# Kernel optimization log

Measured on AMD Instinct MI355X. Metric: run time of the kernel, lower is better.

## Reference

```python
import jax, jax.numpy as jnp
import numpy as np

B, T, N, E, H, L, K = 2, 32, 256, 1024, 16, 2, 256
MAXLEN = 512  # RelativeMultiheadAttention max_seq_len default
SCALES = (1, 2, 4)
TAU = 1.0


def setup_inputs() -> dict:
    key = jax.random.key(0)
    ks = jax.random.split(key, 9)
    s = 0.02
    A = 2 * L  # [layer0-spatial, layer0-temporal, layer1-spatial, layer1-temporal]
    return {
        "x": jax.random.normal(ks[0], (B, T, N, E), jnp.float32),
        "attn_wq": jax.random.normal(ks[1], (A, E, E), jnp.float32) * s,
        "attn_bq": jnp.zeros((A, E), jnp.float32),
        "attn_wk": jax.random.normal(ks[2], (A, E, E), jnp.float32) * s,
        "attn_bk": jnp.zeros((A, E), jnp.float32),
        "attn_wv": jax.random.normal(ks[3], (A, E, E), jnp.float32) * s,
        "attn_bv": jnp.zeros((A, E), jnp.float32),
        "attn_wd": jax.random.normal(ks[4], (A, E, E), jnp.float32) * s,
        "attn_bd": jnp.zeros((A, E), jnp.float32),
        "rel_bias": jax.random.normal(ks[5], (A, 2 * MAXLEN - 1, H), jnp.float32) * s,
        "sel_w": jax.random.normal(ks[6], (E, K), jnp.float32) * s,
        "sel_b": jnp.zeros((K,), jnp.float32),
    }


def _rel_attn(x, wq, bq, wk, bk, wv, bv, wd, bd, rb):
    # x: [Bx, S, E]; rb: [2*MAXLEN-1, H]
    Bx, S, _ = x.shape
    D = E // H
    q = (x @ wq + bq).reshape(Bx, S, H, D)
    k = (x @ wk + bk).reshape(Bx, S, H, D)
    v = (x @ wv + bv).reshape(Bx, S, H, D)
    scores = jnp.einsum('bshd,bthd->bhst', q, k) / jnp.sqrt(jnp.asarray(D, x.dtype))
    pos = jnp.arange(S)
    idx = pos[None, :] - pos[:, None] + (MAXLEN - 1)  # [S, S]
    bias = rb[idx]  # [S, S, H] gathered relative-position bias
    scores = scores + bias.transpose(2, 0, 1)[None]
    w = jax.nn.softmax(scores, axis=-1)
    ctx = jnp.einsum('bhst,bthd->bshd', w, v).reshape(Bx, S, E)
    return ctx @ wd + bd


def reference(x, attn_wq, attn_bq, attn_wk, attn_bk, attn_wv, attn_bv,
              attn_wd, attn_bd, rel_bias, sel_w, sel_b):
    h = x
    for l in range(L):
        # spatial attention over tokens within each frame
        i = 2 * l
        hs = h.reshape(B * T, N, E)
        hs = _rel_attn(hs, attn_wq[i], attn_bq[i], attn_wk[i], attn_bk[i],
                       attn_wv[i], attn_bv[i], attn_wd[i], attn_bd[i], rel_bias[i])
        # temporal attention across frames per spatial location
        j = 2 * l + 1
        ht = hs.reshape(B, T, N, E).transpose(0, 2, 1, 3).reshape(B * N, T, E)
        ht = _rel_attn(ht, attn_wq[j], attn_bq[j], attn_wk[j], attn_bk[j],
                       attn_wv[j], attn_bv[j], attn_wd[j], attn_bd[j], rel_bias[j])
        h = ht.reshape(B, N, T, E).transpose(0, 2, 1, 3)
    # DifferentiableTokenSelection: softmax-weighted pooling into K tokens
    flat = h.reshape(B, T * N, E)
    sc = flat @ sel_w + sel_b  # [B, T*N, K]
    wts = jax.nn.softmax(sc / TAU, axis=1)
    sel = jnp.einsum('bmk,bme->bke', wts, flat)  # [B, K, E]
    # multi-scale average pooling (kernel==stride==scale), concat along tokens
    outs = [sel.reshape(B, K // s, s, E).mean(axis=2) for s in SCALES]
    return jnp.concatenate(outs, axis=1)  # [B, K + K//2 + K//4, E]
```

## Files before the change

### kernel.cpp

```cpp
#include <hip/hip_runtime.h>
#include <stdint.h>


using f16x8 = __attribute__((ext_vector_type(8))) _Float16;
using f16x4 = __attribute__((ext_vector_type(4))) _Float16;
using f32x4 = __attribute__((ext_vector_type(4))) float;

__device__ __forceinline__ int tmap_dev(int m) {
    int bx = m >> 5;
    int s  = m & 31;
    int b  = bx >> 8;
    int n  = bx & 255;
    return (((b << 5) + s) << 8) + n;
}

__device__ __forceinline__ void load16(const _Float16* g, _Float16* l)
{
    __builtin_amdgcn_global_load_lds(
        (const __attribute__((address_space(1))) unsigned int*)g,
        (__attribute__((address_space(3))) unsigned int*)l,
        16, 0, 0);
}

__device__ __forceinline__ void split_f16(float v, _Float16& h, _Float16& l)
{
    h = (_Float16)v;
    l = (_Float16)(v - (float)h);
}

__global__ __launch_bounds__(256)
void conv_act(const float* __restrict__ src, _Float16* __restrict__ dh,
              _Float16* __restrict__ dl, int m_off)
{
    int idx = blockIdx.x * 256 + threadIdx.x;
    int e = idx << 3;
    int ml = e >> 10, col = e & 1023;
    const float* s = src + (size_t)(m_off + ml) * 1024 + col;
    float4 a = *(const float4*)s;
    float4 b = *(const float4*)(s + 4);
    float vv[8] = {a.x, a.y, a.z, a.w, b.x, b.y, b.z, b.w};
    f16x8 vh, vl;
    #pragma unroll
    for (int r = 0; r < 8; r++) {
        _Float16 h, l;
        split_f16(vv[r], h, l);
        vh[r] = h; vl[r] = l;
    }
    *(f16x8*)(dh + (size_t)ml * 1024 + col) = vh;
    *(f16x8*)(dl + (size_t)ml * 1024 + col) = vl;
}

__global__ __launch_bounds__(256)
void conv_wT(const float* __restrict__ W, _Float16* __restrict__ Th,
             _Float16* __restrict__ Tl, int ncols)
{
    __shared__ float Ls[64][65];
    const int n0 = blockIdx.x * 64, k0 = blockIdx.y * 64;
    const int t = threadIdx.x;
    const int kk = t >> 4, nn = (t & 15) << 2;
    #pragma unroll
    for (int i = 0; i < 4; i++) {
        float4 v = *(const float4*)(W + (size_t)(k0 + kk + 16 * i) * ncols + n0 + nn);
        Ls[kk + 16 * i][nn + 0] = v.x; Ls[kk + 16 * i][nn + 1] = v.y;
        Ls[kk + 16 * i][nn + 2] = v.z; Ls[kk + 16 * i][nn + 3] = v.w;
    }
    __syncthreads();
    const int nl = t >> 4, kc = (t & 15) << 2;
    #pragma unroll
    for (int i = 0; i < 4; i++) {
        int n = nl + 16 * i;
        f16x4 hh, ll;
        #pragma unroll
        for (int c = 0; c < 4; c++) {
            _Float16 h, l;
            split_f16(Ls[kc + c][n], h, l);
            hh[c] = h; ll[c] = l;
        }
        *(f16x4*)(Th + (size_t)(n0 + n) * 1024 + k0 + kc) = hh;
        *(f16x4*)(Tl + (size_t)(n0 + n) * 1024 + k0 + kc) = ll;
    }
}

template<int EPI>
__device__ __forceinline__ void gemm_core(
    const _Float16* __restrict__ Ah, const _Float16* __restrict__ Al,
    const _Float16* __restrict__ Wh, const _Float16* __restrict__ Wl,
    const float* __restrict__ bias,
    float* __restrict__ C, _Float16* __restrict__ Ch, _Float16* __restrict__ Cl,
    int ldc, int map_in, int m_off_in, int map_out, int m_off_out,
    int n0, int m0)
{
    __shared__ uint32_t smem_u[8512];
    _Float16* smem = (_Float16*)smem_u;
    _Float16* sAh = smem;
    _Float16* sAl = smem + 4096;
    _Float16* sBh = smem + 8192;
    _Float16* sBl = smem + 12288;

    const int tid = threadIdx.x;
    const int lane = tid & 63;
    const int wv = tid >> 6;
    const int fm = (wv >> 1) << 6;
    const int fn = (wv & 1) << 6;
    const int lm = lane & 15, lq = lane >> 4;

    f32x4 acc[4][4] = {};

    const int srow = tid >> 2;
    const int skc  = (tid & 3) << 3;
    const int gm0 = m_off_in + m0 + srow;
    const int gm1 = gm0 + 64;
    const int r0 = map_in ? tmap_dev(gm0) : gm0;
    const int r1 = map_in ? tmap_dev(gm1) : gm1;
    const _Float16* gAh0 = Ah + (size_t)r0 * 1024 + skc;
    const _Float16* gAh1 = Ah + (size_t)r1 * 1024 + skc;
    const _Float16* gAl0 = Al + (size_t)r0 * 1024 + skc;
    const _Float16* gAl1 = Al + (size_t)r1 * 1024 + skc;
    const _Float16* gB0 = Wh + (size_t)(n0 + srow) * 1024 + skc;
    const _Float16* gB1 = Wl + (size_t)(n0 + srow) * 1024 + skc;
    const int lo = tid << 3;

    for (int k0 = 0; k0 < 1024; k0 += 32) {
        load16(gAh0 + k0, sAh + lo);
        load16(gAh1 + k0, sAh + lo + 2048);
        load16(gAl0 + k0, sAl + lo);
        load16(gAl1 + k0, sAl + lo + 2048);
        load16(gB0 + k0,         sBh + lo);
        load16(gB0 + k0 + 65536, sBh + lo + 2048);
        load16(gB1 + k0,         sBl + lo);
        load16(gB1 + k0 + 65536, sBl + lo + 2048);
        __syncthreads();

        f16x8 ah[4], al[4], bh[4], bl[4];
        #pragma unroll
        for (int i = 0; i < 4; i++) {
            int ra = (fm + i * 16 + lm) * 32 + lq * 8;
            ah[i] = *(const f16x8*)(sAh + ra);
            al[i] = *(const f16x8*)(sAl + ra);
            int rb_ = (fn + i * 16 + lm) * 32 + lq * 8;
            bh[i] = *(const f16x8*)(sBh + rb_);
            bl[i] = *(const f16x8*)(sBl + rb_);
        }
        #pragma unroll
        for (int i = 0; i < 4; i++)
            #pragma unroll
            for (int j = 0; j < 4; j++) {
                acc[i][j] = __builtin_amdgcn_mfma_f32_16x16x32_f16(ah[i], bh[j], acc[i][j], 0, 0, 0);
                acc[i][j] = __builtin_amdgcn_mfma_f32_16x16x32_f16(ah[i], bl[j], acc[i][j], 0, 0, 0);
                acc[i][j] = __builtin_amdgcn_mfma_f32_16x16x32_f16(al[i], bh[j], acc[i][j], 0, 0, 0);
            }
        __syncthreads();
    }

    if (EPI == 0 || EPI == 1) {
        #pragma unroll
        for (int j = 0; j < 4; j++) {
            int n = n0 + fn + j * 16 + lm;
            float bb = bias[n];
            #pragma unroll
            for (int i = 0; i < 4; i++) {
                #pragma unroll
                for (int r = 0; r < 4; r++) {
                    int gm = m_off_out + m0 + fm + i * 16 + lq * 4 + r;
                    int row = map_out ? tmap_dev(gm) : gm;
                    float v = acc[i][j][r] + bb;
                    if (EPI == 0) {
                        C[(size_t)row * ldc + n] = v;
                    } else {
                        _Float16 h, l;
                        split_f16(v, h, l);
                        Ch[(size_t)row * 1024 + n] = h;
                        Cl[(size_t)row * 1024 + n] = l;
                    }
                }
            }
        }
    } else {
        const int fmh = fm >> 6;
        #pragma unroll
        for (int mh = 0; mh < 2; mh++) {
            __syncthreads();
            if (fmh == mh) {
                #pragma unroll
                for (int j = 0; j < 4; j++) {
                    int n = fn + j * 16 + lm;
                    float bb = bias[n0 + n];
                    #pragma unroll
                    for (int i = 0; i < 4; i++) {
                        #pragma unroll
                        for (int r = 0; r < 4; r++) {
                            float v = acc[i][j][r] + bb;
                            _Float16 h, l;
                            split_f16(v, h, l);
                            uint32_t ph = (uint32_t)__builtin_bit_cast(unsigned short, h);
                            uint32_t pl = (uint32_t)__builtin_bit_cast(unsigned short, l);
                            smem_u[(i * 16 + lq * 4 + r) * 133 + n] = ph | (pl << 16);
                        }
                    }
                }
            }
            __syncthreads();
            #pragma unroll
            for (int g = 0; g < 8; g++) {
                int u = tid + g * 256;
                int nn = u >> 4;
                int mg = (u & 15) << 2;
                uint32_t p0 = smem_u[(mg + 0) * 133 + nn];
                uint32_t p1 = smem_u[(mg + 1) * 133 + nn];
                uint32_t p2 = smem_u[(mg + 2) * 133 + nn];
                uint32_t p3 = smem_u[(mg + 3) * 133 + nn];
                f16x4 hh, ll;
                hh[0] = __builtin_bit_cast(_Float16, (unsigned short)(p0 & 0xffff));
                hh[1] = __builtin_bit_cast(_Float16, (unsigned short)(p1 & 0xffff));
                hh[2] = __builtin_bit_cast(_Float16, (unsigned short)(p2 & 0xffff));
                hh[3] = __builtin_bit_cast(_Float16, (unsigned short)(p3 & 0xffff));
                ll[0] = __builtin_bit_cast(_Float16, (unsigned short)(p0 >> 16));
                ll[1] = __builtin_bit_cast(_Float16, (unsigned short)(p1 >> 16));
                ll[2] = __builtin_bit_cast(_Float16, (unsigned short)(p2 >> 16));
                ll[3] = __builtin_bit_cast(_Float16, (unsigned short)(p3 >> 16));
                size_t off = (size_t)(n0 + nn) * 8192 + (m0 + mh * 64 + mg);
                *(f16x4*)(Ch + off) = hh;
                *(f16x4*)(Cl + off) = ll;
            }
        }
    }
}

__global__ __launch_bounds__(256, 2)
void gemm_f16s_f32(const _Float16* __restrict__ Ah, const _Float16* __restrict__ Al,
                   int map_in, int m_off_in,
                   const _Float16* __restrict__ Wh, const _Float16* __restrict__ Wl,
                   const float* __restrict__ bias, float* __restrict__ C, int ldc,
                   int map_out, int m_off_out)
{
    gemm_core<0>(Ah, Al, Wh, Wl, bias, C, nullptr, nullptr, ldc,
                 map_in, m_off_in, map_out, m_off_out,
                 blockIdx.x * 128, blockIdx.y * 128);
}

__global__ __launch_bounds__(256, 2)
void gemm_f16s_h(const _Float16* __restrict__ Ah, const _Float16* __restrict__ Al,
                 int map_in, int m_off_in,
                 const _Float16* __restrict__ Wh, const _Float16* __restrict__ Wl,
                 const float* __restrict__ bias,
                 _Float16* __restrict__ Ch, _Float16* __restrict__ Cl,
                 int map_out, int m_off_out)
{
    gemm_core<1>(Ah, Al, Wh, Wl, bias, nullptr, Ch, Cl, 1024,
                 map_in, m_off_in, map_out, m_off_out,
                 blockIdx.x * 128, blockIdx.y * 128);
}

__global__ __launch_bounds__(256, 2)
void gemm_qkvsplit(const _Float16* __restrict__ Ah, const _Float16* __restrict__ Al,
                   int map_in, int m_off_in,
                   const _Float16* __restrict__ WTh, const _Float16* __restrict__ WTl,
                   const float* __restrict__ bq, const float* __restrict__ bk,
                   const float* __restrict__ bv,
                   _Float16* __restrict__ Qh, _Float16* __restrict__ Ql,
                   _Float16* __restrict__ Kh, _Float16* __restrict__ Kl,
                   _Float16* __restrict__ VTh, _Float16* __restrict__ VTl)
{
    const int z = blockIdx.z;
    const _Float16* wh = WTh + (size_t)z * 1048576;
    const _Float16* wl = WTl + (size_t)z * 1048576;
    if (z == 0)
        gemm_core<1>(Ah, Al, wh, wl, bq, nullptr, Qh, Ql, 1024,
                     map_in, m_off_in, 0, 0, blockIdx.x * 128, blockIdx.y * 128);
    else if (z == 1)
        gemm_core<1>(Ah, Al, wh, wl, bk, nullptr, Kh, Kl, 1024,
                     map_in, m_off_in, 0, 0, blockIdx.x * 128, blockIdx.y * 128);
    else
        gemm_core<3>(Ah, Al, wh, wl, bv, nullptr, VTh, VTl, 0,
                     map_in, m_off_in, 0, 0, blockIdx.x * 128, blockIdx.y * 128);
}

__global__ __launch_bounds__(256, 2)
void attn_s_m(const _Float16* __restrict__ Qh, const _Float16* __restrict__ Ql,
              const _Float16* __restrict__ Kh, const _Float16* __restrict__ Kl,
              const _Float16* __restrict__ VTh, const _Float16* __restrict__ VTl,
              const float* __restrict__ RB,
              _Float16* __restrict__ Ch, _Float16* __restrict__ Cl)
{
    __shared__ _Float16 sKh[2048], sKl[2048];
    __shared__ _Float16 sVh[2560], sVl[2560];
    __shared__ _Float16 sPh[4][2560], sPl[4][2560];
    __shared__ float Bt[512];

    const int tid = threadIdx.x;
    const int lane = tid & 63;
    const int w = tid >> 6;
    const int lm = lane & 15, lq = lane >> 4;
    const int frame = blockIdx.x;
    const int h = blockIdx.y;
    const int rowbase = frame * 256;

    #pragma unroll
    for (int l = 0; l < 2; l++) {
        int idx = tid + l * 256;
        if (idx < 511) Bt[idx] = RB[(size_t)(256 + idx) * 16 + h];
    }

    f16x8 qbh[4][2], qbl[4][2];
    #pragma unroll
    for (int st = 0; st < 4; st++)
        #pragma unroll
        for (int kk = 0; kk < 2; kk++) {
            size_t qo = (size_t)(rowbase + w * 64 + st * 16 + lm) * 1024
                        + h * 64 + kk * 32 + lq * 8;
            qbh[st][kk] = *(const f16x8*)(Qh + qo);
            qbl[st][kk] = *(const f16x8*)(Ql + qo);
        }

    f32x4 cacc[4][4] = {};
    float lsum[4] = {0.f, 0.f, 0.f, 0.f};
    _Float16* Ph = sPh[w];
    _Float16* Pl = sPl[w];

    const int skrow = tid >> 3, skd = (tid & 7) << 3;
    const int svrow = tid >> 2, svj = (tid & 3) << 3;

    for (int jc = 0; jc < 8; jc++) {
        __syncthreads();
        {
            size_t ko = (size_t)(rowbase + jc * 32 + skrow) * 1024 + h * 64 + skd;
            *(f16x8*)(sKh + skrow * 64 + skd) = *(const f16x8*)(Kh + ko);
            *(f16x8*)(sKl + skrow * 64 + skd) = *(const f16x8*)(Kl + ko);
            size_t vo = (size_t)(h * 64 + svrow) * 8192 + rowbase + jc * 32 + svj;
            *(f16x8*)(sVh + svrow * 40 + svj) = *(const f16x8*)(VTh + vo);
            *(f16x8*)(sVl + svrow * 40 + svj) = *(const f16x8*)(VTl + vo);
        }
        __syncthreads();

        f32x4 sacc[2][4] = {};
        #pragma unroll
        for (int jt = 0; jt < 2; jt++) {
            f16x8 kah[2], kal[2];
            #pragma unroll
            for (int kk = 0; kk < 2; kk++) {
                int ra = (jt * 16 + lm) * 64 + kk * 32 + lq * 8;
                kah[kk] = *(const f16x8*)(sKh + ra);
                kal[kk] = *(const f16x8*)(sKl + ra);
            }
            #pragma unroll
            for (int st = 0; st < 4; st++)
                #pragma unroll
                for (int kk = 0; kk < 2; kk++) {
                    sacc[jt][st] = __builtin_amdgcn_mfma_f32_16x16x32_f16(kah[kk], qbh[st][kk], sacc[jt][st], 0, 0, 0);
                    sacc[jt][st] = __builtin_amdgcn_mfma_f32_16x16x32_f16(kah[kk], qbl[st][kk], sacc[jt][st], 0, 0, 0);
                    sacc[jt][st] = __builtin_amdgcn_mfma_f32_16x16x32_f16(kal[kk], qbh[st][kk], sacc[jt][st], 0, 0, 0);
                }
        }

        #pragma unroll
        for (int jt = 0; jt < 2; jt++)
            #pragma unroll
            for (int st = 0; st < 4; st++) {
                f16x4 p4h, p4l;
                #pragma unroll
                for (int r = 0; r < 4; r++) {
                    int j = jc * 32 + jt * 16 + lq * 4 + r;
                    int s = w * 64 + st * 16 + lm;
                    float p = __expf(sacc[jt][st][r] * 0.125f + Bt[j - s + 255]);
                    lsum[st] += p;
                    _Float16 hp, lp;
                    split_f16(p, hp, lp);
                    p4h[r] = hp; p4l[r] = lp;
                }
                int pa = (st * 16 + lm) * 40 + jt * 16 + lq * 4;
                *(f16x4*)(Ph + pa) = p4h;
                *(f16x4*)(Pl + pa) = p4l;
            }

        #pragma unroll
        for (int st = 0; st < 4; st++) {
            int pb = (st * 16 + lm) * 40 + lq * 8;
            f16x8 pbh = *(const f16x8*)(Ph + pb);
            f16x8 pbl = *(const f16x8*)(Pl + pb);
            #pragma unroll
            for (int dt = 0; dt < 4; dt++) {
                int va = (dt * 16 + lm) * 40 + lq * 8;
                f16x8 vah = *(const f16x8*)(sVh + va);
                f16x8 val = *(const f16x8*)(sVl + va);
                cacc[dt][st] = __builtin_amdgcn_mfma_f32_16x16x32_f16(vah, pbh, cacc[dt][st], 0, 0, 0);
                cacc[dt][st] = __builtin_amdgcn_mfma_f32_16x16x32_f16(vah, pbl, cacc[dt][st], 0, 0, 0);
                cacc[dt][st] = __builtin_amdgcn_mfma_f32_16x16x32_f16(val, pbh, cacc[dt][st], 0, 0, 0);
            }
        }
    }

    float inv[4];
    #pragma unroll
    for (int st = 0; st < 4; st++) {
        float t = lsum[st];
        t += __shfl_xor(t, 16);
        t += __shfl_xor(t, 32);
        inv[st] = 1.0f / t;
    }

    #pragma unroll
    for (int st = 0; st < 4; st++)
        #pragma unroll
        for (int dt = 0; dt < 4; dt++) {
            f16x4 oh, ol;
            #pragma unroll
            for (int r = 0; r < 4; r++) {
                _Float16 hp, lp;
                split_f16(cacc[dt][st][r] * inv[st], hp, lp);
                oh[r] = hp; ol[r] = lp;
            }
            size_t oo = (size_t)(rowbase + w * 64 + st * 16 + lm) * 1024
                        + h * 64 + dt * 16 + lq * 4;
            *(f16x4*)(Ch + oo) = oh;
            *(f16x4*)(Cl + oo) = ol;
        }
}

__global__ __launch_bounds__(256, 2)
void attn_t_m(const _Float16* __restrict__ Qh, const _Float16* __restrict__ Ql,
              const _Float16* __restrict__ Kh, const _Float16* __restrict__ Kl,
              const _Float16* __restrict__ VTh, const _Float16* __restrict__ VTl,
              const float* __restrict__ RB,
              _Float16* __restrict__ Ch, _Float16* __restrict__ Cl)
{
    __shared__ _Float16 sPh[4][1280], sPl[4][1280];
    __shared__ float Bt[64];

    const int tid = threadIdx.x;
    const int lane = tid & 63;
    const int w = tid >> 6;
    const int lm = lane & 15, lq = lane >> 4;
    const int h = blockIdx.y;
    const int bx = blockIdx.x * 4 + w;
    const int rowbase = bx * 32;

    if (tid < 63) Bt[tid] = RB[(size_t)(480 + tid) * 16 + h];
    __syncthreads();

    f16x8 qbh[2][2], qbl[2][2];
    #pragma unroll
    for (int st = 0; st < 2; st++)
        #pragma unroll
        for (int kk = 0; kk < 2; kk++) {
            size_t qo = (size_t)(rowbase + st * 16 + lm) * 1024 + h * 64 + kk * 32 + lq * 8;
            qbh[st][kk] = *(const f16x8*)(Qh + qo);
            qbl[st][kk] = *(const f16x8*)(Ql + qo);
        }

    f32x4 sacc[2][2] = {};
    #pragma unroll
    for (int jt = 0; jt < 2; jt++) {
        f16x8 kah[2], kal[2];
        #pragma unroll
        for (int kk = 0; kk < 2; kk++) {
            size_t ko = (size_t)(rowbase + jt * 16 + lm) * 1024 + h * 64 + kk * 32 + lq * 8;
            kah[kk] = *(const f16x8*)(Kh + ko);
            kal[kk] = *(const f16x8*)(Kl + ko);
        }
        #pragma unroll
        for (int st = 0; st < 2; st++)
            #pragma unroll
            for (int kk = 0; kk < 2; kk++) {
                sacc[jt][st] = __builtin_amdgcn_mfma_f32_16x16x32_f16(kah[kk], qbh[st][kk], sacc[jt][st], 0, 0, 0);
                sacc[jt][st] = __builtin_amdgcn_mfma_f32_16x16x32_f16(kah[kk], qbl[st][kk], sacc[jt][st], 0, 0, 0);
                sacc[jt][st] = __builtin_amdgcn_mfma_f32_16x16x32_f16(kal[kk], qbh[st][kk], sacc[jt][st], 0, 0, 0);
            }
    }

    float lsum[2] = {0.f, 0.f};
    _Float16* Ph = sPh[w];
    _Float16* Pl = sPl[w];
    #pragma unroll
    for (int jt = 0; jt < 2; jt++)
        #pragma unroll
        for (int st = 0; st < 2; st++) {
            f16x4 p4h, p4l;
            #pragma unroll
            for (int r = 0; r < 4; r++) {
                int j = jt * 16 + lq * 4 + r;
                int s = st * 16 + lm;
                float p = __expf(sacc[jt][st][r] * 0.125f + Bt[j - s + 31]);
                lsum[st] += p;
                _Float16 hp, lp;
                split_f16(p, hp, lp);
                p4h[r] = hp; p4l[r] = lp;
            }
            int pa = (st * 16 + lm) * 40 + jt * 16 + lq * 4;
            *(f16x4*)(Ph + pa) = p4h;
            *(f16x4*)(Pl + pa) = p4l;
        }

    f16x8 vah[4], val[4];
    #pragma unroll
    for (int dt = 0; dt < 4; dt++) {
        size_t vo = (size_t)(h * 64 + dt * 16 + lm) * 8192 + rowbase + lq * 8;
        vah[dt] = *(const f16x8*)(VTh + vo);
        val[dt] = *(const f16x8*)(VTl + vo);
    }
    f32x4 cacc[4][2] = {};
    #pragma unroll
    for (int st = 0; st < 2; st++) {
        int pb = (st * 16 + lm) * 40 + lq * 8;
        f16x8 pbh = *(const f16x8*)(Ph + pb);
        f16x8 pbl = *(const f16x8*)(Pl + pb);
        #pragma unroll
        for (int dt = 0; dt < 4; dt++) {
            cacc[dt][st] = __builtin_amdgcn_mfma_f32_16x16x32_f16(vah[dt], pbh, cacc[dt][st], 0, 0, 0);
            cacc[dt][st] = __builtin_amdgcn_mfma_f32_16x16x32_f16(vah[dt], pbl, cacc[dt][st], 0, 0, 0);
            cacc[dt][st] = __builtin_amdgcn_mfma_f32_16x16x32_f16(val[dt], pbh, cacc[dt][st], 0, 0, 0);
        }
    }

    float inv[2];
    #pragma unroll
    for (int st = 0; st < 2; st++) {
        float t = lsum[st];
        t += __shfl_xor(t, 16);
        t += __shfl_xor(t, 32);
        inv[st] = 1.0f / t;
    }

    #pragma unroll
    for (int st = 0; st < 2; st++)
        #pragma unroll
        for (int dt = 0; dt < 4; dt++) {
            f16x4 oh, ol;
            #pragma unroll
            for (int r = 0; r < 4; r++) {
                _Float16 hp, lp;
                split_f16(cacc[dt][st][r] * inv[st], hp, lp);
                oh[r] = hp; ol[r] = lp;
            }
            size_t oo = (size_t)(rowbase + st * 16 + lm) * 1024 + h * 64 + dt * 16 + lq * 4;
            *(f16x4*)(Ch + oo) = oh;
            *(f16x4*)(Cl + oo) = ol;
        }
}

__global__ __launch_bounds__(256)
void colsum_part_kernel(const float* __restrict__ SC, float* __restrict__ P)
{
    int bid = blockIdx.x;
    int b = bid >> 7, chunk = bid & 127;
    int base = b * 8192 + chunk * 64;
    int k = threadIdx.x;
    float sum = 0.0f;
    for (int r = 0; r < 64; r++)
        sum += __expf(SC[(size_t)(base + r) * 256 + k]);
    P[(size_t)bid * 256 + k] = sum;
}

__global__ __launch_bounds__(256)
void colsum_reduce_kernel(const float* __restrict__ P, float* __restrict__ CS)
{
    int b = blockIdx.x;
    int k = threadIdx.x;
    float s = 0.0f;
    for (int c = 0; c < 128; c++)
        s += P[(size_t)(b * 128 + c) * 256 + k];
    CS[b * 256 + k] = s;
}

__global__ __launch_bounds__(256)
void trans_wts(const float* __restrict__ SC, const float* __restrict__ CS,
               _Float16* __restrict__ Th, _Float16* __restrict__ Tl)
{
    __shared__ float L[64][65];
    const int mt = blockIdx.x * 64;
    const int kt = blockIdx.y * 64;
    const int b  = mt >> 13;
    const int ml = mt & 8191;
    const int tid = threadIdx.x;
    #pragma unroll
    for (int l = 0; l < 4; l++) {
        int idx = tid + 256 * l;
        int r = idx >> 4, c4 = (idx & 15) << 2;
        float4 v = *(const float4*)(SC + (size_t)(mt + r) * 256 + kt + c4);
        L[r][c4 + 0] = __expf(v.x); L[r][c4 + 1] = __expf(v.y);
        L[r][c4 + 2] = __expf(v.z); L[r][c4 + 3] = __expf(v.w);
    }
    __syncthreads();
    #pragma unroll
    for (int l = 0; l < 4; l++) {
        int idx = tid + 256 * l;
        int rk = idx >> 4, c4 = (idx & 15) << 2;
        float inv = 1.0f / CS[b * 256 + kt + rk];
        f16x4 hh, ll;
        #pragma unroll
        for (int u = 0; u < 4; u++) {
            _Float16 h, l2;
            split_f16(L[c4 + u][rk] * inv, h, l2);
            hh[u] = h; ll[u] = l2;
        }
        size_t o = ((size_t)b * 256 + kt + rk) * 8192 + ml + c4;
        *(f16x4*)(Th + o) = hh;
        *(f16x4*)(Tl + o) = ll;
    }
}

__global__ __launch_bounds__(256)
void trans_f16(const _Float16* __restrict__ Sh, const _Float16* __restrict__ Sl,
               _Float16* __restrict__ Th, _Float16* __restrict__ Tl)
{
    __shared__ _Float16 L[64][72];
    const int mt = blockIdx.x * 64, et = blockIdx.y * 64;
    const _Float16* S = blockIdx.z ? Sl : Sh;
    _Float16* T = blockIdx.z ? Tl : Th;
    const int tid = threadIdx.x;
    #pragma unroll
    for (int l = 0; l < 2; l++) {
        int v = tid * 2 + l;
        int r = v >> 3, c8 = (v & 7) << 3;
        *(f16x8*)&L[r][c8] = *(const f16x8*)(S + (size_t)(mt + r) * 1024 + et + c8);
    }
    __syncthreads();
    #pragma unroll
    for (int l = 0; l < 2; l++) {
        int v = tid * 2 + l;
        int r = v >> 3, c8 = (v & 7) << 3;
        f16x8 o;
        #pragma unroll
        for (int u = 0; u < 8; u++) o[u] = L[c8 + u][r];
        *(f16x8*)(T + (size_t)(et + r) * 16384 + mt + c8) = o;
    }
}

__global__ __launch_bounds__(256, 2)
void gemm_selm(const _Float16* __restrict__ Wth, const _Float16* __restrict__ Wtl,
               const _Float16* __restrict__ Hth, const _Float16* __restrict__ Htl,
               float* __restrict__ P)
{
    __shared__ _Float16 sAh[4096], sAl[4096], sBh[4096], sBl[4096];
    const int tid = threadIdx.x;
    const int lane = tid & 63;
    const int wv = tid >> 6;
    const int fm = (wv >> 1) << 6;
    const int fn = (wv & 1) << 6;
    const int lm = lane & 15, lq = lane >> 4;
    const int n0 = blockIdx.x * 128;
    const int m0 = blockIdx.y * 128;
    const int z  = blockIdx.z;
    const int b = z >> 3, sp = z & 7;

    f32x4 acc[4][4] = {};

    const int srow = tid >> 2;
    const int skc  = (tid & 3) << 3;
    const _Float16* gAh0 = Wth + ((size_t)b * 256 + m0 + srow) * 8192 + sp * 1024 + skc;
    const _Float16* gAl0 = Wtl + ((size_t)b * 256 + m0 + srow) * 8192 + sp * 1024 + skc;
    const _Float16* gB0 = Hth + (size_t)(n0 + srow) * 16384 + b * 8192 + sp * 1024 + skc;
    const _Float16* gB1 = Htl + (size_t)(n0 + srow) * 16384 + b * 8192 + sp * 1024 + skc;
    const int lo = tid << 3;

    for (int k0 = 0; k0 < 1024; k0 += 32) {
        load16(gAh0 + k0,          sAh + lo);
        load16(gAh0 + k0 + 524288, sAh + lo + 2048);
        load16(gAl0 + k0,          sAl + lo);
        load16(gAl0 + k0 + 524288, sAl + lo + 2048);
        load16(gB0 + k0,           sBh + lo);
        load16(gB0 + k0 + 1048576, sBh + lo + 2048);
        load16(gB1 + k0,           sBl + lo);
        load16(gB1 + k0 + 1048576, sBl + lo + 2048);
        __syncthreads();

        f16x8 ah[4], al[4], bh[4], bl[4];
        #pragma unroll
        for (int i = 0; i < 4; i++) {
            int ra = (fm + i * 16 + lm) * 32 + lq * 8;
            ah[i] = *(const f16x8*)(sAh + ra);
            al[i] = *(const f16x8*)(sAl + ra);
            int rb_ = (fn + i * 16 + lm) * 32 + lq * 8;
            bh[i] = *(const f16x8*)(sBh + rb_);
            bl[i] = *(const f16x8*)(sBl + rb_);
        }
        #pragma unroll
        for (int i = 0; i < 4; i++)
            #pragma unroll
            for (int j = 0; j < 4; j++) {
                acc[i][j] = __builtin_amdgcn_mfma_f32_16x16x32_f16(ah[i], bh[j], acc[i][j], 0, 0, 0);
                acc[i][j] = __builtin_amdgcn_mfma_f32_16x16x32_f16(ah[i], bl[j], acc[i][j], 0, 0, 0);
                acc[i][j] = __builtin_amdgcn_mfma_f32_16x16x32_f16(al[i], bh[j], acc[i][j], 0, 0, 0);
            }
        __syncthreads();
    }

    float* Pz = P + (size_t)z * 262144;
    #pragma unroll
    for (int j = 0; j < 4; j++) {
        int n = n0 + fn + j * 16 + lm;
        #pragma unroll
        for (int i = 0; i < 4; i++)
            #pragma unroll
            for (int r = 0; r < 4; r++) {
                int k = m0 + fm + i * 16 + lq * 4 + r;
                Pz[(size_t)k * 1024 + n] = acc[i][j][r];
            }
    }
}

__global__ __launch_bounds__(256)
void sel_reduce(const float* __restrict__ P, float* __restrict__ SEL)
{
    int idx4 = blockIdx.x * 256 + threadIdx.x;
    int e = idx4 << 2;
    int b = e >> 18;
    int rest = e & 262143;
    const float* p = P + (size_t)(b * 8) * 262144 + rest;
    float4 acc = {0.f, 0.f, 0.f, 0.f};
    #pragma unroll
    for (int s = 0; s < 8; s++) {
        float4 v = *(const float4*)(p + (size_t)s * 262144);
        acc.x += v.x; acc.y += v.y; acc.z += v.z; acc.w += v.w;
    }
    *(float4*)(SEL + e) = acc;
}

__global__ __launch_bounds__(256)
void pool_kernel(const float* __restrict__ SEL, float* __restrict__ out)
{
    int i4 = blockIdx.x * 256 + threadIdx.x;
    int e  = i4 << 2;
    int row = e >> 10;
    int b = row / 448;
    int r = row - b * 448;
    int c = e & 1023;
    const float* sb = SEL + (size_t)b * (256 * 1024);
    float4 o;
    if (r < 256) {
        o = *(const float4*)(sb + (size_t)r * 1024 + c);
    } else if (r < 384) {
        int r2 = (r - 256) * 2;
        float4 x0 = *(const float4*)(sb + (size_t)r2 * 1024 + c);
        float4 x1 = *(const float4*)(sb + (size_t)(r2 + 1) * 1024 + c);
        o.x = 0.5f * (x0.x + x1.x); o.y = 0.5f * (x0.y + x1.y);
        o.z = 0.5f * (x0.z + x1.z); o.w = 0.5f * (x0.w + x1.w);
    } else {
        int r4 = (r - 384) * 4;
        float4 x0 = *(const float4*)(sb + (size_t)(r4 + 0) * 1024 + c);
        float4 x1 = *(const float4*)(sb + (size_t)(r4 + 1) * 1024 + c);
        float4 x2 = *(const float4*)(sb + (size_t)(r4 + 2) * 1024 + c);
        float4 x3 = *(const float4*)(sb + (size_t)(r4 + 3) * 1024 + c);
        o.x = 0.25f * (x0.x + x1.x + x2.x + x3.x);
        o.y = 0.25f * (x0.y + x1.y + x2.y + x3.y);
        o.z = 0.25f * (x0.z + x1.z + x2.z + x3.z);
        o.w = 0.25f * (x0.w + x1.w + x2.w + x3.w);
    }
    *(float4*)(out + e) = o;
}

extern "C" void kernel_launch(void* const* d_in, const int* in_sizes, int n_in,
                              void* d_out, int out_size, void* d_ws, size_t ws_size,
                              hipStream_t stream)
{
    const float* x    = (const float*)d_in[0];
    const float* wq   = (const float*)d_in[1];
    const float* bq   = (const float*)d_in[2];
    const float* wk   = (const float*)d_in[3];
    const float* bk   = (const float*)d_in[4];
    const float* wv   = (const float*)d_in[5];
    const float* bv   = (const float*)d_in[6];
    const float* wd   = (const float*)d_in[7];
    const float* bd   = (const float*)d_in[8];
    const float* rb   = (const float*)d_in[9];
    const float* selw = (const float*)d_in[10];
    const float* selb = (const float*)d_in[11];
    float* out = (float*)d_out;

    float* base = (float*)d_ws;
    _Float16* Hh  = (_Float16*)base;
    _Float16* Hl  = Hh + 16777216;
    _Float16* Qh  = (_Float16*)(base + 16777216);
    _Float16* Ql  = Qh + 8388608;
    _Float16* Kh  = Ql + 8388608;
    _Float16* Kl  = Kh + 8388608;
    _Float16* VTh = (_Float16*)(base + 33554432);
    _Float16* VTl = VTh + 8388608;
    _Float16* CXh = (_Float16*)(base + 41943040);
    _Float16* CXl = CXh + 8388608;
    _Float16* WTh = (_Float16*)(base + 50331648);
    _Float16* WTl = WTh + 4194304;
    _Float16* Ah  = (_Float16*)(base + 54525952);
    _Float16* Al  = Ah + 8388608;
    float* SC   = (float*)Qh;
    float* Pp   = (float*)Kh;
    float* SEL  = (float*)Kl;
    float* PART = SEL + 524288;
    float* CSUM = PART + 65536;
    _Float16* WTTh = CXh;
    _Float16* WTTl = CXl;
    _Float16* HTh  = Ah;
    _Float16* HTl  = VTh;

    const dim3 blk(256);

    for (int a = 0; a < 4; a++) {
        const int mi = (a & 1);
        const size_t wo = (size_t)a * 1048576;
        const int bo = a * 1024;
        const float* rba = rb + (size_t)a * 1023 * 16;

        conv_wT<<<dim3(16, 16), blk, 0, stream>>>(wq + wo, WTh,           WTl,           1024);
        conv_wT<<<dim3(16, 16), blk, 0, stream>>>(wk + wo, WTh + 1048576, WTl + 1048576, 1024);
        conv_wT<<<dim3(16, 16), blk, 0, stream>>>(wv + wo, WTh + 2097152, WTl + 2097152, 1024);
        conv_wT<<<dim3(16, 16), blk, 0, stream>>>(wd + wo, WTh + 3145728, WTl + 3145728, 1024);

        for (int c = 0; c < 2; c++) {
            const int mo = c * 8192;
            const _Float16 *sH, *sL;
            int sm, so;
            if (a == 0) {
                conv_act<<<4096, blk, 0, stream>>>(x, Ah, Al, mo);
                sH = Ah; sL = Al; sm = 0; so = 0;
            } else {
                sH = Hh; sL = Hl; sm = mi; so = mo;
            }
            gemm_qkvsplit<<<dim3(8, 64, 3), blk, 0, stream>>>(
                sH, sL, sm, so, WTh, WTl, bq + bo, bk + bo, bv + bo,
                Qh, Ql, Kh, Kl, VTh, VTl);
            if (mi == 0)
                attn_s_m<<<dim3(32, 16), blk, 0, stream>>>(Qh, Ql, Kh, Kl, VTh, VTl, rba, CXh, CXl);
            else
                attn_t_m<<<dim3(64, 16), blk, 0, stream>>>(Qh, Ql, Kh, Kl, VTh, VTl, rba, CXh, CXl);
            gemm_f16s_h<<<dim3(8, 64), blk, 0, stream>>>(
                CXh, CXl, 0, 0, WTh + 3145728, WTl + 3145728, bd + bo, Hh, Hl, mi, mo);
        }
    }

    conv_wT<<<dim3(4, 16), blk, 0, stream>>>(selw, WTh, WTl, 256);
    gemm_f16s_f32<<<dim3(2, 128), blk, 0, stream>>>(
        Hh, Hl, 0, 0, WTh, WTl, selb, SC, 256, 0, 0);
    colsum_part_kernel<<<256, blk, 0, stream>>>(SC, PART);
    colsum_reduce_kernel<<<2, blk, 0, stream>>>(PART, CSUM);
    trans_wts<<<dim3(256, 4), blk, 0, stream>>>(SC, CSUM, WTTh, WTTl);
    trans_f16<<<dim3(256, 16, 2), blk, 0, stream>>>(Hh, Hl, HTh, HTl);
    gemm_selm<<<dim3(8, 2, 16), blk, 0, stream>>>(WTTh, WTTl, HTh, HTl, Pp);
    sel_reduce<<<512, blk, 0, stream>>>(Pp, SEL);
    pool_kernel<<<896, blk, 0, stream>>>(SEL, out);
}
```

Measured before the change: 2.507 ms.

## Use 256x128 GEMM tiles with 512 threads, triple buffering, and swizzled block order

Replaces the 128x128 split-fp16 GEMMs used for the QKV and output projections with a new 256x128 tile core run by 512 threads (8 waves). The core uses three-stage global-to-LDS pipelining with XOR-swizzled LDS layout and s_setprio around the MFMA blocks. A 1D grid with a remapped block index groups tiles for better L2 reuse of the A and W panels. The larger tile cuts redundant A/W loads per output, at the cost of much more LDS per block (144KB), which may limit occupancy to one block per CU despite launch_bounds(512,2).

Result: faster. 2.124 ms (-15.3%).

```diff
diff --git a/kernel.cpp b/kernel.cpp
--- a/kernel.cpp
+++ b/kernel.cpp
@@ -238,41 +238,208 @@
                  blockIdx.x * 128, blockIdx.y * 128);
 }
 
-__global__ __launch_bounds__(256, 2)
-void gemm_f16s_h(const _Float16* __restrict__ Ah, const _Float16* __restrict__ Al,
+template<int EPI>
+__device__ __forceinline__ void gemm256_core(
+    uint32_t* __restrict__ smem_u,
+    const _Float16* __restrict__ Ah, const _Float16* __restrict__ Al,
+    const _Float16* __restrict__ Wh, const _Float16* __restrict__ Wl,
+    const float* __restrict__ bias,
+    _Float16* __restrict__ Ch, _Float16* __restrict__ Cl,
+    int map_in, int m_off_in, int map_out, int m_off_out,
+    int n0, int m0)
+{
+    _Float16* S = (_Float16*)smem_u;
+    const int tid  = threadIdx.x;
+    const int lane = tid & 63;
+    const int wv = tid >> 6;
+    const int wm = wv >> 1;
+    const int fm = wm << 6;
+    const int fn = (wv & 1) << 6;
+    const int lm = lane & 15, lq = lane >> 4;
+    const int ko = ((lq ^ ((lm >> 1) & 3)) << 3);
+
+    f32x4 acc[4][4] = {};
+
+    const int srow = tid >> 2;
+    const int scol = (((tid & 3) ^ ((tid >> 3) & 3)) << 3);
+    const int gm0 = m_off_in + m0 + srow;
+    const int gm1 = gm0 + 128;
+    const int r0 = map_in ? tmap_dev(gm0) : gm0;
+    const int r1 = map_in ? tmap_dev(gm1) : gm1;
+    const _Float16* gAh0 = Ah + (size_t)r0 * 1024 + scol;
+    const _Float16* gAh1 = Ah + (size_t)r1 * 1024 + scol;
+    const _Float16* gAl0 = Al + (size_t)r0 * 1024 + scol;
+    const _Float16* gAl1 = Al + (size_t)r1 * 1024 + scol;
+    const _Float16* gBh  = Wh + (size_t)(n0 + srow) * 1024 + scol;
+    const _Float16* gBl  = Wl + (size_t)(n0 + srow) * 1024 + scol;
+    const int lo = tid << 3;
+
+    auto stage = [&](int t, int b) {
+        const int k0 = t << 5;
+        _Float16* d = S + b * 24576;
+        load16(gAh0 + k0, d + lo);
+        load16(gAh1 + k0, d + 4096  + lo);
+        load16(gAl0 + k0, d + 8192  + lo);
+        load16(gAl1 + k0, d + 12288 + lo);
+        load16(gBh  + k0, d + 16384 + lo);
+        load16(gBl  + k0, d + 20480 + lo);
+    };
+
+    auto kstep = [&](int t, int cb, int sb, bool last) {
+        if (last) asm volatile("s_waitcnt vmcnt(0) lgkmcnt(0)" ::: "memory");
+        else      asm volatile("s_waitcnt vmcnt(6) lgkmcnt(0)" ::: "memory");
+        __builtin_amdgcn_s_barrier();
+        if (sb >= 0) stage(t + 2, sb);
+
+        const _Float16* c = S + cb * 24576;
+        f16x8 ah[4], al[4], bh[4], bl[4];
+        #pragma unroll
+        for (int i = 0; i < 4; i++) {
+            int ra = (fm + i * 16 + lm) * 32 + ko;
+            ah[i] = *(const f16x8*)(c + ra);
+            al[i] = *(const f16x8*)(c + 8192 + ra);
+            int rb = (fn + i * 16 + lm) * 32 + ko;
+            bh[i] = *(const f16x8*)(c + 16384 + rb);
+            bl[i] = *(const f16x8*)(c + 20480 + rb);
+        }
+        __builtin_amdgcn_s_setprio(1);
+        #pragma unroll
+        for (int i = 0; i < 4; i++)
+            #pragma unroll
+            for (int j = 0; j < 4; j++) {
+                acc[i][j] = __builtin_amdgcn_mfma_f32_16x16x32_f16(ah[i], bh[j], acc[i][j], 0, 0, 0);
+                acc[i][j] = __builtin_amdgcn_mfma_f32_16x16x32_f16(ah[i], bl[j], acc[i][j], 0, 0, 0);
+                acc[i][j] = __builtin_amdgcn_mfma_f32_16x16x32_f16(al[i], bh[j], acc[i][j], 0, 0, 0);
+            }
+        __builtin_amdgcn_s_setprio(0);
+    };
+
+    stage(0, 0);
+    stage(1, 1);
+    #pragma unroll 1
+    for (int tt = 0; tt < 30; tt += 3) {
+        kstep(tt + 0, 0, 2, false);
+        kstep(tt + 1, 1, 0, false);
+        kstep(tt + 2, 2, 1, false);
+    }
+    kstep(30, 0, -1, false);
+    kstep(31, 1, -1, true);
+
+    if (EPI == 1) {
+        #pragma unroll
+        for (int j = 0; j < 4; j++) {
+            int n = n0 + fn + j * 16 + lm;
+            float bb = bias[n];
+            #pragma unroll
+            for (int i = 0; i < 4; i++) {
+                #pragma unroll
+                for (int r = 0; r < 4; r++) {
+                    int gm = m_off_out + m0 + fm + i * 16 + lq * 4 + r;
+                    int row = map_out ? tmap_dev(gm) : gm;
+                    float v = acc[i][j][r] + bb;
+                    _Float16 h, l;
+                    split_f16(v, h, l);
+                    Ch[(size_t)row * 1024 + n] = h;
+                    Cl[(size_t)row * 1024 + n] = l;
+                }
+            }
+        }
+    } else {
+        #pragma unroll 1
+        for (int q = 0; q < 4; q++) {
+            __syncthreads();
+            if (wm == q) {
+                #pragma unroll
+                for (int j = 0; j < 4; j++) {
+                    int ncol = fn + j * 16 + lm;
+                    float bb = bias[n0 + ncol];
+                    #pragma unroll
+                    for (int i = 0; i < 4; i++) {
+                        #pragma unroll
+                        for (int r = 0; r < 4; r++) {
+                            float v = acc[i][j][r] + bb;
+                            _Float16 h, l;
+                            split_f16(v, h, l);
+                            uint32_t ph = (uint32_t)__builtin_bit_cast(unsigned short, h);
+                            uint32_t pl = (uint32_t)__builtin_bit_cast(unsigned short, l);
+                            smem_u[(i * 16 + lq * 4 + r) * 129 + ncol] = ph | (pl << 16);
+                        }
+                    }
+                }
+            }
+            __syncthreads();
+            #pragma unroll
+            for (int g = 0; g < 4; g++) {
+                int u = tid + g * 512;
+                int nn = u >> 4;
+                int mg = (u & 15) << 2;
+                uint32_t p0 = smem_u[(mg + 0) * 129 + nn];
+                uint32_t p1 = smem_u[(mg + 1) * 129 + nn];
+                uint32_t p2 = smem_u[(mg + 2) * 129 + nn];
+                uint32_t p3 = smem_u[(mg + 3) * 129 + nn];
+                f16x4 hh, ll;
+                hh[0] = __builtin_bit_cast(_Float16, (unsigned short)(p0 & 0xffff));
+                hh[1] = __builtin_bit_cast(_Float16, (unsigned short)(p1 & 0xffff));
+                hh[2] = __builtin_bit_cast(_Float16, (unsigned short)(p2 & 0xffff));
+                hh[3] = __builtin_bit_cast(_Float16, (unsigned short)(p3 & 0xffff));
+                ll[0] = __builtin_bit_cast(_Float16, (unsigned short)(p0 >> 16));
+                ll[1] = __builtin_bit_cast(_Float16, (unsigned short)(p1 >> 16));
+                ll[2] = __builtin_bit_cast(_Float16, (unsigned short)(p2 >> 16));
+                ll[3] = __builtin_bit_cast(_Float16, (unsigned short)(p3 >> 16));
+                size_t off = (size_t)(n0 + nn) * 8192 + (m0 + q * 64 + mg);
+                *(f16x4*)(Ch + off) = hh;
+                *(f16x4*)(Cl + off) = ll;
+            }
+        }
+    }
+}
+
+__global__ __launch_bounds__(512, 2)
+void gemm_qkv256(const _Float16* __restrict__ Ah, const _Float16* __restrict__ Al,
                  int map_in, int m_off_in,
-                 const _Float16* __restrict__ Wh, const _Float16* __restrict__ Wl,
-                 const float* __restrict__ bias,
-                 _Float16* __restrict__ Ch, _Float16* __restrict__ Cl,
-                 int map_out, int m_off_out)
-{
-    gemm_core<1>(Ah, Al, Wh, Wl, bias, nullptr, Ch, Cl, 1024,
-                 map_in, m_off_in, map_out, m_off_out,
-                 blockIdx.x * 128, blockIdx.y * 128);
-}
-
-__global__ __launch_bounds__(256, 2)
-void gemm_qkvsplit(const _Float16* __restrict__ Ah, const _Float16* __restrict__ Al,
-                   int map_in, int m_off_in,
-                   const _Float16* __restrict__ WTh, const _Float16* __restrict__ WTl,
-                   const float* __restrict__ bq, const float* __restrict__ bk,
-                   const float* __restrict__ bv,
-                   _Float16* __restrict__ Qh, _Float16* __restrict__ Ql,
-                   _Float16* __restrict__ Kh, _Float16* __restrict__ Kl,
-                   _Float16* __restrict__ VTh, _Float16* __restrict__ VTl)
-{
-    const int z = blockIdx.z;
+                 const _Float16* __restrict__ WTh, const _Float16* __restrict__ WTl,
+                 const float* __restrict__ bq, const float* __restrict__ bk,
+                 const float* __restrict__ bv,
+                 _Float16* __restrict__ Qh, _Float16* __restrict__ Ql,
+                 _Float16* __restrict__ Kh, _Float16* __restrict__ Kl,
+                 _Float16* __restrict__ VTh, _Float16* __restrict__ VTl)
+{
+    __shared__ uint32_t smem_u[36864];
+    const int bid = blockIdx.x;
+    const int wg = (bid & 7) * 96 + (bid >> 3);
+    const int z = wg >> 8;
+    const int rem = wg & 255;
+    const int m0 = (rem >> 3) << 8;
+    const int n0 = (rem & 7) << 7;
     const _Float16* wh = WTh + (size_t)z * 1048576;
     const _Float16* wl = WTl + (size_t)z * 1048576;
-    if (z == 0)
-        gemm_core<1>(Ah, Al, wh, wl, bq, nullptr, Qh, Ql, 1024,
-                     map_in, m_off_in, 0, 0, blockIdx.x * 128, blockIdx.y * 128);
-    else if (z == 1)
-        gemm_core<1>(Ah, Al, wh, wl, bk, nullptr, Kh, Kl, 1024,
-                     map_in, m_off_in, 0, 0, blockIdx.x * 128, blockIdx.y * 128);
-    else
-        gemm_core<3>(Ah, Al, wh, wl, bv, nullptr, VTh, VTl, 0,
-                     map_in, m_off_in, 0, 0, blockIdx.x * 128, blockIdx.y * 128);
+    if (z < 2) {
+        const float* bb = (z == 0) ? bq : bk;
+        _Float16* oh = (z == 0) ? Qh : Kh;
+        _Float16* ol = (z == 0) ? Ql : Kl;
+        gemm256_core<1>(smem_u, Ah, Al, wh, wl, bb, oh, ol,
+                        map_in, m_off_in, 0, 0, n0, m0);
+    } else {
+        gemm256_core<3>(smem_u, Ah, Al, wh, wl, bv, VTh, VTl,
+                        map_in, m_off_in, 0, 0, n0, m0);
+    }
+}
+
+__global__ __launch_bounds__(512, 2)
+void gemm_h256(const _Float16* __restrict__ Ah, const _Float16* __restrict__ Al,
+               int map_in, int m_off_in,
+               const _Float16* __restrict__ Wh, const _Float16* __restrict__ Wl,
+               const float* __restrict__ bias,
+               _Float16* __restrict__ Ch, _Float16* __restrict__ Cl,
+               int map_out, int m_off_out)
+{
+    __shared__ uint32_t smem_u[36864];
+    const int bid = blockIdx.x;
+    const int wg = (bid & 7) * 32 + (bid >> 3);
+    const int m0 = (wg >> 3) << 8;
+    const int n0 = (wg & 7) << 7;
+    gemm256_core<1>(smem_u, Ah, Al, Wh, Wl, bias, Ch, Cl,
+                    map_in, m_off_in, map_out, m_off_out, n0, m0);
 }
 
 __global__ __launch_bounds__(256, 2)
@@ -792,6 +959,7 @@
     _Float16* HTl  = VTh;
 
     const dim3 blk(256);
+    const dim3 blk2(512);
 
     for (int a = 0; a < 4; a++) {
         const int mi = (a & 1);
@@ -814,14 +982,14 @@
             } else {
                 sH = Hh; sL = Hl; sm = mi; so = mo;
             }
-            gemm_qkvsplit<<<dim3(8, 64, 3), blk, 0, stream>>>(
+            gemm_qkv256<<<dim3(768), blk2, 0, stream>>>(
                 sH, sL, sm, so, WTh, WTl, bq + bo, bk + bo, bv + bo,
                 Qh, Ql, Kh, Kl, VTh, VTl);
             if (mi == 0)
                 attn_s_m<<<dim3(32, 16), blk, 0, stream>>>(Qh, Ql, Kh, Kl, VTh, VTl, rba, CXh, CXl);
             else
                 attn_t_m<<<dim3(64, 16), blk, 0, stream>>>(Qh, Ql, Kh, Kl, VTh, VTl, rba, CXh, CXl);
-            gemm_f16s_h<<<dim3(8, 64), blk, 0, stream>>>(
+            gemm_h256<<<dim3(256), blk2, 0, stream>>>(
                 CXh, CXl, 0, 0, WTh + 3145728, WTl + 3145728, bd + bo, Hh, Hl, mi, mo);
         }
     }
```
